# Kernel optimization log

Measured on AMD Instinct MI355X. Metric: run time of the kernel, lower is better.

The kernel has to match this reference:

```python
import jax, jax.numpy as jnp
import numpy as np

N_EVENTS = 16384
B = 4
H = W = 64
KH = KW = 3
P = KH * KW
D = 256  # input_size == hidden_size


def setup_inputs() -> dict:
    rng = np.random.default_rng(0)
    # events sorted by batch, time = arange (sorted within batch)
    batch_id = np.sort(rng.integers(0, B, N_EVENTS))
    hh = rng.integers(KH - 1, H - KH + 1, N_EVENTS)  # interior pixels -> exactly P patches each
    ww = rng.integers(KW - 1, W - KW + 1, N_EVENTS)
    time = np.arange(N_EVENTS)
    # scatter each event to its P=kh*kw overlapping patches (stride 1)
    Hp, Wp = H - KH + 1, W - KW + 1
    ki = np.arange(KH)[:, None]
    kj = np.arange(KW)[None, :]
    pos = (ki * KW + kj).reshape(1, P)                       # [1, P]
    pl = hh[:, None] - ki.reshape(1, -1).repeat(KW, 1).reshape(1, P) if False else None
    ki_f = np.repeat(np.arange(KH), KW)                       # [P]
    kj_f = np.tile(np.arange(KW), KH)                         # [P]
    patch_row = hh[:, None] - ki_f[None, :]                   # [N, P]
    patch_col = ww[:, None] - kj_f[None, :]
    patch_lin = (batch_id[:, None] * (Hp * Wp) + patch_row * Wp + patch_col).reshape(-1)
    pos_flat = np.broadcast_to((ki_f * KW + kj_f)[None, :], (N_EVENTS, P)).reshape(-1)
    orig_flat = np.repeat(np.arange(N_EVENTS), P)
    t_flat = np.repeat(time, P)
    order = np.lexsort((t_flat, patch_lin))                   # group by patch, time-ordered within
    patch_sorted = patch_lin[order]
    orig_event_idx = orig_flat[order].astype(np.int32)
    pos_id = pos_flat[order].astype(np.int32)
    seg_start = np.concatenate([[True], patch_sorted[1:] != patch_sorted[:-1]])

    key = jax.random.key(0)
    ks = jax.random.split(key, 8)
    std = np.sqrt(2.0 / (D + D)).astype(np.float32)
    lin = 1.0 / np.sqrt(D).astype(np.float32)
    return {
        "events": jax.random.normal(ks[0], (N_EVENTS, D), jnp.float32),
        "scatter_w": jax.random.normal(ks[1], (P, D, D), jnp.float32) * std,
        "gather_w": jax.random.normal(ks[2], (P, D, D), jnp.float32) * std,
        "q_w": jax.random.normal(ks[3], (D, D), jnp.float32) * lin,
        "v_w": jax.random.normal(ks[4], (D, D), jnp.float32) * lin,
        "g_w": jax.random.normal(ks[5], (D, D), jnp.float32) * lin,
        "o_w": jax.random.normal(ks[6], (D, D), jnp.float32) * lin,
        "ln_gamma": jnp.ones((D,), jnp.float32),
        "ln_beta": jnp.zeros((D,), jnp.float32),
        "orig_event_idx": jnp.asarray(orig_event_idx),
        "pos_id": jnp.asarray(pos_id),
        "seg_start": jnp.asarray(seg_start),
    }


def _pos_proj(x, weights, pos_id):
    # per-patch-position linear: out[n] = weights[pos_id[n]] @ x[n]
    # disjoint masks partition rows, so masked GEMMs sum exactly (mirrors torch loop)
    out = jnp.zeros((x.shape[0], weights.shape[1]), x.dtype)
    for i in range(weights.shape[0]):
        m = (pos_id == i)[:, None]
        out = out + jnp.where(m, x @ weights[i].T, 0.0)
    return out


def _gated_scan(g, v, seg_start):
    # h_t = g_t * h_{t-1} + (1 - g_t) * v_t, reset at segment starts
    a = jnp.where(seg_start[:, None], 0.0, g)
    b = (1.0 - g) * v
    def comb(c1, c2):
        a1, b1 = c1
        a2, b2 = c2
        return (a1 * a2, a2 * b1 + b2)
    _, h = jax.lax.associative_scan(comb, (a, b), axis=0)
    return h


def reference(events, scatter_w, gather_w, q_w, v_w, g_w, o_w, ln_gamma, ln_beta,
              orig_event_idx, pos_id, seg_start):
    x = events[orig_event_idx]                     # [M, D] scatter events -> patch copies
    y = _pos_proj(x, scatter_w, pos_id)            # indexed conv-like projection
    q = y @ q_w.T
    v = y @ v_w.T
    g = jax.nn.sigmoid(y @ g_w.T)
    h = _gated_scan(g, v, seg_start)               # ragged gated linear scan
    o = (q * h) @ o_w.T
    z = _pos_proj(o, gather_w, pos_id)             # indexed gather projection
    out = jnp.zeros_like(events).at[orig_event_idx].add(z)  # gather back (sum over P copies)
    out = out + events                             # residual (input_size == hidden_size)
    mu = jnp.mean(out, axis=-1, keepdims=True)
    var = jnp.mean(jnp.square(out - mu), axis=-1, keepdims=True)
    out = (out - mu) * jax.lax.rsqrt(var + 1e-5) * ln_gamma + ln_beta
    return out
```

## Files before the change

kernel.cpp:

```cpp
#include <hip/hip_runtime.h>

typedef __bf16 bf16x8 __attribute__((ext_vector_type(8)));
typedef float f32x4 __attribute__((ext_vector_type(4)));

#define NEV 16384
#define MTOT 147456
#define LDQ 2304
#define WSZ 37748736L

__device__ __forceinline__ unsigned short f2bf(float f) {
  unsigned x = __float_as_uint(f);
  x += 0x7FFFu + ((x >> 16) & 1u);
  return (unsigned short)(x >> 16);
}
__device__ __forceinline__ float bf2f(unsigned short u) {
  return __uint_as_float(((unsigned)u) << 16);
}
__device__ __forceinline__ void load_lds16(const void* g, void* l) {
  __builtin_amdgcn_global_load_lds(
      (const __attribute__((address_space(1))) unsigned int*)g,
      (__attribute__((address_space(3))) unsigned int*)l, 16, 0, 0);
}

__global__ void k_cast4(const float* __restrict__ in, unsigned short* __restrict__ out, int n4) {
  int i = blockIdx.x * blockDim.x + threadIdx.x;
  if (i >= n4) return;
  float4 v = reinterpret_cast<const float4*>(in)[i];
  ushort4 o;
  o.x = f2bf(v.x); o.y = f2bf(v.y); o.z = f2bf(v.z); o.w = f2bf(v.w);
  reinterpret_cast<ushort4*>(out)[i] = o;
}

__global__ void k_cast3(const float* __restrict__ q, const float* __restrict__ v,
                        const float* __restrict__ g, unsigned short* __restrict__ out) {
  int which = blockIdx.y;
  const float* src = (which == 0) ? q : (which == 1) ? v : g;
  int i = blockIdx.x * blockDim.x + threadIdx.x;
  if (i >= 16384) return;
  float4 val = reinterpret_cast<const float4*>(src)[i];
  ushort4 o;
  o.x = f2bf(val.x); o.y = f2bf(val.y); o.z = f2bf(val.z); o.w = f2bf(val.w);
  reinterpret_cast<ushort4*>(out + (long)which * 65536)[i] = o;
}

__global__ void k_transpose(const float* __restrict__ in, unsigned short* __restrict__ out, int total) {
  int i = blockIdx.x * blockDim.x + threadIdx.x;
  if (i >= total) return;
  int b = i >> 16, r = (i >> 8) & 255, c = i & 255;
  out[i] = f2bf(in[((long)b << 16) + (c << 8) + r]);
}

__global__ void k_detect(const unsigned int* __restrict__ seg, int* mode) {
  __shared__ int fFloat, fGt1;
  if (threadIdx.x == 0) { fFloat = 0; fGt1 = 0; }
  __syncthreads();
  int lf = 0, lg = 0;
  for (int i = threadIdx.x; i < 1024; i += 256) {
    unsigned v = seg[i];
    if (v == 0x3F800000u) lf = 1;
    else if (v > 1u) lg = 1;
  }
  if (lf) atomicOr(&fFloat, 1);
  if (lg) atomicOr(&fGt1, 1);
  __syncthreads();
  if (threadIdx.x == 0) *mode = fFloat ? 2 : (fGt1 ? 1 : 0);
}

__device__ __forceinline__ bool is_start(const void* seg, int mode, int i) {
  if (mode == 1) return ((const unsigned char*)seg)[i] != 0;
  if (mode == 2) return ((const float*)seg)[i] != 0.0f;
  return ((const int*)seg)[i] != 0;
}

__global__ void k_compact(const void* __restrict__ seg, const int* __restrict__ mode,
                          int* counter, int* starts) {
  int i = blockIdx.x * blockDim.x + threadIdx.x;
  if (i >= MTOT) return;
  if (is_start(seg, *mode, i)) {
    int k = atomicAdd(counter, 1);
    starts[k] = i;
  }
}

template<bool F32OUT>
__device__ __forceinline__ void gemm_tile(
    const unsigned short* __restrict__ A, const unsigned short* __restrict__ B,
    void* __restrict__ Cv, int r0, int c0, int K, int lda, int ldb, int ldc,
    unsigned short* As, unsigned short* Bs) {
  const int tid = threadIdx.x, lane = tid & 63, wid = tid >> 6;
  const int wr = (wid >> 1) * 64, wc = (wid & 1) * 64;
  const int la = lane & 15, lb2 = lane >> 4;
  const int arow = tid >> 2;
  const int cs = ((tid & 3) ^ ((arow >> 1) & 3)) * 8;
  const int nk = K >> 5;
  f32x4 acc[4][4];
#pragma unroll
  for (int i = 0; i < 4; ++i)
#pragma unroll
    for (int j = 0; j < 4; ++j) acc[i][j] = (f32x4)0.0f;

  const unsigned short* ga0 = A + (long)(r0 + arow) * lda + cs;
  const unsigned short* gb0 = B + (long)(c0 + arow) * ldb + cs;

  load_lds16(ga0, &As[tid * 8]);
  load_lds16(ga0 + (long)64 * lda, &As[2048 + tid * 8]);
  load_lds16(gb0, &Bs[tid * 8]);
  load_lds16(gb0 + (long)64 * ldb, &Bs[2048 + tid * 8]);
  __syncthreads();

  for (int k = 0; k < nk; ++k) {
    if (k + 1 < nk) {
      const int nb = ((k + 1) & 1) * 4096;
      const unsigned short* ga = ga0 + (k + 1) * 32;
      const unsigned short* gb = gb0 + (k + 1) * 32;
      load_lds16(ga, &As[nb + tid * 8]);
      load_lds16(ga + (long)64 * lda, &As[nb + 2048 + tid * 8]);
      load_lds16(gb, &Bs[nb + tid * 8]);
      load_lds16(gb + (long)64 * ldb, &Bs[nb + 2048 + tid * 8]);
    }
    const int cb = (k & 1) * 4096;
    bf16x8 af[4], bv[4];
#pragma unroll
    for (int i = 0; i < 4; ++i) {
      const int ra = wr + i * 16 + la;
      const int rb = wc + i * 16 + la;
      af[i] = *reinterpret_cast<const bf16x8*>(&As[cb + ra * 32 + ((lb2 ^ ((ra >> 1) & 3)) * 8)]);
      bv[i] = *reinterpret_cast<const bf16x8*>(&Bs[cb + rb * 32 + ((lb2 ^ ((rb >> 1) & 3)) * 8)]);
    }
#pragma unroll
    for (int i = 0; i < 4; ++i)
#pragma unroll
      for (int j = 0; j < 4; ++j)
        acc[i][j] = __builtin_amdgcn_mfma_f32_16x16x32_bf16(af[i], bv[j], acc[i][j], 0, 0, 0);
    __syncthreads();
  }
#pragma unroll
  for (int i = 0; i < 4; ++i)
#pragma unroll
    for (int j = 0; j < 4; ++j)
#pragma unroll
      for (int r = 0; r < 4; ++r) {
        const int row = r0 + wr + i * 16 + lb2 * 4 + r;
        const int col = c0 + wc + j * 16 + la;
        if (F32OUT) ((float*)Cv)[(long)row * ldc + col] = acc[i][j][r];
        else ((unsigned short*)Cv)[(long)row * ldc + col] = f2bf(acc[i][j][r]);
      }
}

__global__ __launch_bounds__(256) void k_wgemm(
    const unsigned short* __restrict__ qvgw, const unsigned short* __restrict__ wt,
    const unsigned short* __restrict__ gaw, const unsigned short* __restrict__ owt,
    unsigned short* __restrict__ ABig, unsigned short* __restrict__ Bo2) {
  __shared__ __align__(16) unsigned short As[8192];
  __shared__ __align__(16) unsigned short Bs[8192];
  const int b = blockIdx.z;
  const unsigned short *A, *B;
  unsigned short* C;
  int ldc;
  if (b < 27) {
    A = qvgw + (long)(b / 9) * 65536;
    B = wt + (long)(b % 9) * 65536;
    C = ABig + (long)b * 65536; ldc = 256;
  } else {
    A = gaw + (long)(b - 27) * 65536;
    B = owt;
    C = Bo2 + (b - 27) * 256; ldc = LDQ;
  }
  gemm_tile<false>(A, B, C, blockIdx.x * 128, blockIdx.y * 128, 256, 256, 256, ldc, As, Bs);
}

__global__ __launch_bounds__(256) void k_qvg(
    const unsigned short* __restrict__ ev, const unsigned short* __restrict__ ABig,
    unsigned short* __restrict__ X) {
  __shared__ __align__(16) unsigned short As[8192];
  __shared__ __align__(16) unsigned short Bs[8192];
  const int b = blockIdx.z;
  const unsigned short* B = ABig + (long)b * 65536;
  unsigned short* C = X + (long)(b / 9) * WSZ + (b % 9) * 256;
  gemm_tile<false>(ev, B, C, blockIdx.x * 128, blockIdx.y * 128, 256, 256, 256, LDQ, As, Bs);
}

__global__ __launch_bounds__(256) void k_scan(
    unsigned short* __restrict__ X,
    const int* __restrict__ starts, const int* __restrict__ cntp, const int* __restrict__ modep,
    const void* __restrict__ seg, const int* __restrict__ pos_id, const int* __restrict__ oidx) {
  const int lane = threadIdx.x & 63;
  const int w = blockIdx.x * 4 + (threadIdx.x >> 6);
  const int nW = gridDim.x * 4;
  const int nseg = *cntp;
  const int md = *modep;
  for (int s = w; s < nseg; s += nW) {
    int t = starts[s];
    int p = pos_id[t], e = oidx[t];
    long base = (long)e * LDQ + p * 256 + lane * 4;
    ushort4 ql = *(const ushort4*)(X + base);
    ushort4 vl = *(const ushort4*)(X + base + WSZ);
    ushort4 gl = *(const ushort4*)(X + base + 2 * WSZ);
    bool cont = (t + 1 < MTOT) && !is_start(seg, md, t + 1);
    float h0 = 0.f, h1 = 0.f, h2 = 0.f, h3 = 0.f;
    for (;;) {
      ushort4 qn, vn, gn;
      long nbase = 0;
      bool cont2 = false;
      if (cont) {
        int pn = pos_id[t + 1], en = oidx[t + 1];
        nbase = (long)en * LDQ + pn * 256 + lane * 4;
        qn = *(const ushort4*)(X + nbase);
        vn = *(const ushort4*)(X + nbase + WSZ);
        gn = *(const ushort4*)(X + nbase + 2 * WSZ);
        cont2 = (t + 2 < MTOT) && !is_start(seg, md, t + 2);
      }
      float g0 = 1.f / (1.f + __expf(-bf2f(gl.x)));
      float g1 = 1.f / (1.f + __expf(-bf2f(gl.y)));
      float g2 = 1.f / (1.f + __expf(-bf2f(gl.z)));
      float g3 = 1.f / (1.f + __expf(-bf2f(gl.w)));
      h0 = g0 * h0 + (1.f - g0) * bf2f(vl.x);
      h1 = g1 * h1 + (1.f - g1) * bf2f(vl.y);
      h2 = g2 * h2 + (1.f - g2) * bf2f(vl.z);
      h3 = g3 * h3 + (1.f - g3) * bf2f(vl.w);
      ushort4 o;
      o.x = f2bf(bf2f(ql.x) * h0);
      o.y = f2bf(bf2f(ql.y) * h1);
      o.z = f2bf(bf2f(ql.z) * h2);
      o.w = f2bf(bf2f(ql.w) * h3);
      *(ushort4*)(X + base + WSZ) = o;
      if (!cont) break;
      ++t;
      base = nbase; ql = qn; vl = vn; gl = gn; cont = cont2;
    }
  }
}

__global__ __launch_bounds__(256) void k_p5(
    const unsigned short* __restrict__ QH, const unsigned short* __restrict__ Bo2,
    float* __restrict__ S) {
  __shared__ __align__(16) unsigned short As[8192];
  __shared__ __align__(16) unsigned short Bs[8192];
  gemm_tile<true>(QH, Bo2, S, blockIdx.x * 128, blockIdx.y * 128, LDQ, LDQ, LDQ, 256, As, Bs);
}

__global__ __launch_bounds__(256) void k_ln(float* __restrict__ S, const float* __restrict__ ev,
                                            const float* __restrict__ gamma, const float* __restrict__ beta) {
  int row = blockIdx.x * 4 + (threadIdx.x >> 6);
  int lane = threadIdx.x & 63;
  long base = (long)row * 256 + lane * 4;
  float4 s4 = *reinterpret_cast<const float4*>(S + base);
  float4 e4 = *reinterpret_cast<const float4*>(ev + base);
  float v0 = s4.x + e4.x, v1 = s4.y + e4.y, v2 = s4.z + e4.z, v3 = s4.w + e4.w;
  float s = v0 + v1 + v2 + v3;
  float ss = v0 * v0 + v1 * v1 + v2 * v2 + v3 * v3;
  for (int o = 32; o; o >>= 1) { s += __shfl_xor(s, o, 64); ss += __shfl_xor(ss, o, 64); }
  float mu = s * (1.0f / 256.0f);
  float var = ss * (1.0f / 256.0f) - mu * mu;
  float rs = rsqrtf(fmaxf(var, 0.0f) + 1e-5f);
  float4 g4 = *reinterpret_cast<const float4*>(gamma + lane * 4);
  float4 b4 = *reinterpret_cast<const float4*>(beta + lane * 4);
  float4 o4;
  o4.x = (v0 - mu) * rs * g4.x + b4.x;
  o4.y = (v1 - mu) * rs * g4.y + b4.y;
  o4.z = (v2 - mu) * rs * g4.z + b4.z;
  o4.w = (v3 - mu) * rs * g4.w + b4.w;
  *reinterpret_cast<float4*>(S + base) = o4;
}

extern "C" void kernel_launch(void* const* d_in, const int* in_sizes, int n_in,
                              void* d_out, int out_size, void* d_ws, size_t ws_size,
                              hipStream_t stream) {
  const float* events    = (const float*)d_in[0];
  const float* scatter_w = (const float*)d_in[1];
  const float* gather_w  = (const float*)d_in[2];
  const float* q_w       = (const float*)d_in[3];
  const float* v_w       = (const float*)d_in[4];
  const float* g_w       = (const float*)d_in[5];
  const float* o_w       = (const float*)d_in[6];
  const float* ln_gamma  = (const float*)d_in[7];
  const float* ln_beta   = (const float*)d_in[8];
  const int*   oidx      = (const int*)d_in[9];
  const int*   pos_id    = (const int*)d_in[10];
  const void*  seg       = d_in[11];
  float* out = (float*)d_out;

  char* base = (char*)d_ws;
  int* counter = (int*)base;
  int* mode    = (int*)(base + 4);
  int* starts  = (int*)(base + 256);
  unsigned short* ev_bf  = (unsigned short*)(base + 590080);
  unsigned short* wt     = (unsigned short*)(base + 8978688);
  unsigned short* qvgw   = (unsigned short*)(base + 10158336);
  unsigned short* owt    = (unsigned short*)(base + 10551552);
  unsigned short* gaw_bf = (unsigned short*)(base + 10682624);
  unsigned short* ABig   = (unsigned short*)(base + 11862272);
  unsigned short* Bo2    = (unsigned short*)(base + 15401216);
  unsigned short* X      = (unsigned short*)(base + 16580864);

  hipMemsetAsync(counter, 0, 8, stream);
  k_detect<<<1, 256, 0, stream>>>((const unsigned int*)seg, mode);

  k_cast4<<<4096, 256, 0, stream>>>(events, ev_bf, 1048576);
  k_cast3<<<dim3(64, 3), 256, 0, stream>>>(q_w, v_w, g_w, qvgw);
  k_cast4<<<576, 256, 0, stream>>>(gather_w, gaw_bf, 147456);
  k_transpose<<<2304, 256, 0, stream>>>(scatter_w, wt, 589824);
  k_transpose<<<256, 256, 0, stream>>>(o_w, owt, 65536);

  k_wgemm<<<dim3(2, 2, 36), 256, 0, stream>>>(qvgw, wt, gaw_bf, owt, ABig, Bo2);

  k_qvg<<<dim3(128, 2, 27), 256, 0, stream>>>(ev_bf, ABig, X);

  k_compact<<<576, 256, 0, stream>>>(seg, mode, counter, starts);
  k_scan<<<2048, 256, 0, stream>>>(X, starts, counter, mode, seg, pos_id, oidx);

  k_p5<<<dim3(128, 2), 256, 0, stream>>>(X + WSZ, Bo2, out);
  k_ln<<<4096, 256, 0, stream>>>(out, events, ln_gamma, ln_beta);
}
```

Measured before the change: 268.2 us.

## Fuse q/v/g event GEMMs to share A tiles and fold residual into epilogue

Replaces the per-weight q/v/g GEMM launch (27 z-slices) with one kernel per position that loads each event tile once and multiplies it against all three weight matrices, using XOR-swizzled 64-wide K tiles and 128x64 output tiles. This cuts redundant A-tile global loads by about a factor of three. The cost is higher accumulator register pressure, which may lower occupancy. Separately, the residual add moves into the f32 epilogue of the final GEMM, so the layernorm kernel no longer reads the events array.

```diff
diff --git a/kernel.cpp b/kernel.cpp
--- a/kernel.cpp
+++ b/kernel.cpp
@@ -85,7 +85,8 @@
 template<bool F32OUT>
 __device__ __forceinline__ void gemm_tile(
     const unsigned short* __restrict__ A, const unsigned short* __restrict__ B,
-    void* __restrict__ Cv, int r0, int c0, int K, int lda, int ldb, int ldc,
+    void* __restrict__ Cv, const float* __restrict__ resid,
+    int r0, int c0, int K, int lda, int ldb, int ldc,
     unsigned short* As, unsigned short* Bs) {
   const int tid = threadIdx.x, lane = tid & 63, wid = tid >> 6;
   const int wr = (wid >> 1) * 64, wc = (wid & 1) * 64;
@@ -142,8 +143,13 @@
       for (int r = 0; r < 4; ++r) {
         const int row = r0 + wr + i * 16 + lb2 * 4 + r;
         const int col = c0 + wc + j * 16 + la;
-        if (F32OUT) ((float*)Cv)[(long)row * ldc + col] = acc[i][j][r];
-        else ((unsigned short*)Cv)[(long)row * ldc + col] = f2bf(acc[i][j][r]);
+        if (F32OUT) {
+          float v = acc[i][j][r];
+          if (resid) v += resid[(long)row * ldc + col];
+          ((float*)Cv)[(long)row * ldc + col] = v;
+        } else {
+          ((unsigned short*)Cv)[(long)row * ldc + col] = f2bf(acc[i][j][r]);
+        }
       }
 }
 
@@ -166,18 +172,86 @@
     B = owt;
     C = Bo2 + (b - 27) * 256; ldc = LDQ;
   }
-  gemm_tile<false>(A, B, C, blockIdx.x * 128, blockIdx.y * 128, 256, 256, 256, ldc, As, Bs);
-}
-
-__global__ __launch_bounds__(256) void k_qvg(
+  gemm_tile<false>(A, B, C, nullptr, blockIdx.x * 128, blockIdx.y * 128, 256, 256, 256, ldc, As, Bs);
+}
+
+__global__ __launch_bounds__(256) void k_qvg3(
     const unsigned short* __restrict__ ev, const unsigned short* __restrict__ ABig,
     unsigned short* __restrict__ X) {
   __shared__ __align__(16) unsigned short As[8192];
-  __shared__ __align__(16) unsigned short Bs[8192];
-  const int b = blockIdx.z;
-  const unsigned short* B = ABig + (long)b * 65536;
-  unsigned short* C = X + (long)(b / 9) * WSZ + (b % 9) * 256;
-  gemm_tile<false>(ev, B, C, blockIdx.x * 128, blockIdx.y * 128, 256, 256, 256, LDQ, As, Bs);
+  __shared__ __align__(16) unsigned short Bs[3][4096];
+  const int p = blockIdx.z;
+  const int r0 = blockIdx.x * 128, c0 = blockIdx.y * 64;
+  const int tid = threadIdx.x, lane = tid & 63, wid = tid >> 6;
+  const int wr2 = (wid >> 1) * 64, wc2 = (wid & 1) * 32;
+  const int la = lane & 15, lb2 = lane >> 4;
+  f32x4 acc[3][4][2];
+#pragma unroll
+  for (int w = 0; w < 3; ++w)
+#pragma unroll
+    for (int i = 0; i < 4; ++i)
+#pragma unroll
+      for (int j = 0; j < 2; ++j) acc[w][i][j] = (f32x4)0.0f;
+
+  for (int k0 = 0; k0 < 256; k0 += 64) {
+#pragma unroll
+    for (int q = 0; q < 4; ++q) {
+      const int g = q * 256 + tid;
+      const int row = g >> 3, c = g & 7;
+      load_lds16(ev + (long)(r0 + row) * 256 + k0 + ((c ^ (row & 7)) * 8), &As[g * 8]);
+    }
+#pragma unroll
+    for (int w = 0; w < 3; ++w) {
+      const unsigned short* Bw = ABig + (long)(w * 9 + p) * 65536;
+#pragma unroll
+      for (int q = 0; q < 2; ++q) {
+        const int g = q * 256 + tid;
+        const int row = g >> 3, c = g & 7;
+        load_lds16(Bw + (long)(c0 + row) * 256 + k0 + ((c ^ (row & 7)) * 8), &Bs[w][g * 8]);
+      }
+    }
+    __syncthreads();
+#pragma unroll
+    for (int kk = 0; kk < 2; ++kk) {
+      bf16x8 af[4], bv[3][2];
+#pragma unroll
+      for (int i = 0; i < 4; ++i) {
+        const int ra = wr2 + i * 16 + la;
+        const int slot = (kk * 4 + lb2) ^ (ra & 7);
+        af[i] = *reinterpret_cast<const bf16x8*>(&As[ra * 64 + slot * 8]);
+      }
+#pragma unroll
+      for (int w = 0; w < 3; ++w)
+#pragma unroll
+        for (int j = 0; j < 2; ++j) {
+          const int rb = wc2 + j * 16 + la;
+          const int slot = (kk * 4 + lb2) ^ (rb & 7);
+          bv[w][j] = *reinterpret_cast<const bf16x8*>(&Bs[w][rb * 64 + slot * 8]);
+        }
+#pragma unroll
+      for (int w = 0; w < 3; ++w)
+#pragma unroll
+        for (int i = 0; i < 4; ++i)
+#pragma unroll
+          for (int j = 0; j < 2; ++j)
+            acc[w][i][j] = __builtin_amdgcn_mfma_f32_16x16x32_bf16(af[i], bv[w][j], acc[w][i][j], 0, 0, 0);
+    }
+    __syncthreads();
+  }
+#pragma unroll
+  for (int w = 0; w < 3; ++w) {
+    unsigned short* Xw = X + (long)w * WSZ + p * 256;
+#pragma unroll
+    for (int i = 0; i < 4; ++i)
+#pragma unroll
+      for (int j = 0; j < 2; ++j)
+#pragma unroll
+        for (int r = 0; r < 4; ++r) {
+          const int row = r0 + wr2 + i * 16 + lb2 * 4 + r;
+          const int col = c0 + wc2 + j * 16 + la;
+          Xw[(long)row * LDQ + col] = f2bf(acc[w][i][j][r]);
+        }
+  }
 }
 
 __global__ __launch_bounds__(256) void k_scan(
@@ -233,20 +307,19 @@
 
 __global__ __launch_bounds__(256) void k_p5(
     const unsigned short* __restrict__ QH, const unsigned short* __restrict__ Bo2,
-    float* __restrict__ S) {
+    const float* __restrict__ ev, float* __restrict__ S) {
   __shared__ __align__(16) unsigned short As[8192];
   __shared__ __align__(16) unsigned short Bs[8192];
-  gemm_tile<true>(QH, Bo2, S, blockIdx.x * 128, blockIdx.y * 128, LDQ, LDQ, LDQ, 256, As, Bs);
-}
-
-__global__ __launch_bounds__(256) void k_ln(float* __restrict__ S, const float* __restrict__ ev,
+  gemm_tile<true>(QH, Bo2, S, ev, blockIdx.x * 128, blockIdx.y * 128, LDQ, LDQ, LDQ, 256, As, Bs);
+}
+
+__global__ __launch_bounds__(256) void k_ln(float* __restrict__ S,
                                             const float* __restrict__ gamma, const float* __restrict__ beta) {
   int row = blockIdx.x * 4 + (threadIdx.x >> 6);
   int lane = threadIdx.x & 63;
   long base = (long)row * 256 + lane * 4;
   float4 s4 = *reinterpret_cast<const float4*>(S + base);
-  float4 e4 = *reinterpret_cast<const float4*>(ev + base);
-  float v0 = s4.x + e4.x, v1 = s4.y + e4.y, v2 = s4.z + e4.z, v3 = s4.w + e4.w;
+  float v0 = s4.x, v1 = s4.y, v2 = s4.z, v3 = s4.w;
   float s = v0 + v1 + v2 + v3;
   float ss = v0 * v0 + v1 * v1 + v2 * v2 + v3 * v3;
   for (int o = 32; o; o >>= 1) { s += __shfl_xor(s, o, 64); ss += __shfl_xor(ss, o, 64); }
@@ -304,11 +377,11 @@
 
   k_wgemm<<<dim3(2, 2, 36), 256, 0, stream>>>(qvgw, wt, gaw_bf, owt, ABig, Bo2);
 
-  k_qvg<<<dim3(128, 2, 27), 256, 0, stream>>>(ev_bf, ABig, X);
+  k_qvg3<<<dim3(128, 4, 9), 256, 0, stream>>>(ev_bf, ABig, X);
 
   k_compact<<<576, 256, 0, stream>>>(seg, mode, counter, starts);
   k_scan<<<2048, 256, 0, stream>>>(X, starts, counter, mode, seg, pos_id, oidx);
 
-  k_p5<<<dim3(128, 2), 256, 0, stream>>>(X + WSZ, Bo2, out);
-  k_ln<<<4096, 256, 0, stream>>>(out, events, ln_gamma, ln_beta);
-}
+  k_p5<<<dim3(128, 2), 256, 0, stream>>>(X + WSZ, Bo2, events, out);
+  k_ln<<<4096, 256, 0, stream>>>(out, ln_gamma, ln_beta);
+}
```

New measurement: 287.8 us. 7.3% more time.
